# Kernel optimization log

Hardware: AMD Instinct MI355X
Metric: run time of the kernel (lower is better)

The kernel has to match this reference:

```python
import jax, jax.numpy as jnp
import numpy as np

N = 100000      # nodes
E = 1600000     # directed edges (avg degree 16)
F_IN = 256      # dataset.num_node_features
HID = 64        # hidden
C = 40          # dataset.num_classes


def setup_inputs() -> dict:
    key = jax.random.key(0)
    k0, k1, k2, k3 = jax.random.split(key, 4)
    x = jax.random.normal(k0, (N, F_IN), dtype=jnp.float32)
    edge_index = jax.random.randint(k1, (2, E), 0, N, dtype=jnp.int32)
    # Glorot-style init like GCNConv.reset_parameters
    W1 = jax.random.normal(k2, (F_IN, HID), dtype=jnp.float32) * (1.0 / np.sqrt(F_IN))
    b1 = jnp.zeros((HID,), dtype=jnp.float32)
    W2 = jax.random.normal(k3, (HID, C), dtype=jnp.float32) * (1.0 / np.sqrt(HID))
    b2 = jnp.zeros((C,), dtype=jnp.float32)
    return {"x": x, "edge_index": edge_index, "W1": W1, "b1": b1, "W2": W2, "b2": b2}


def gcn_conv(x, row, col, norm, W, b):
    # PyG GCNConv: out[col] += norm * (x @ W)[row]; then + bias
    n = x.shape[0]
    h = x @ W                                   # [N, out]
    msg = h[row] * norm[:, None]                # [E+N, out] gather + scale
    out = jax.ops.segment_sum(msg, col, num_segments=n)  # scatter-add
    return out + b


def _norm_coeffs(edge_index, n, dtype):
    # add self-loops, then symmetric normalization D^{-1/2} A D^{-1/2}
    loop = jnp.arange(n, dtype=edge_index.dtype)
    row = jnp.concatenate([edge_index[0], loop])
    col = jnp.concatenate([edge_index[1], loop])
    deg = jax.ops.segment_sum(jnp.ones_like(col, dtype=dtype), col, num_segments=n)
    dis = jnp.where(deg > 0, jax.lax.rsqrt(jnp.maximum(deg, 1.0)), 0.0)
    return row, col, dis[row] * dis[col]


def reference(x, edge_index, W1, b1, W2, b2):
    n = x.shape[0]
    row, col, norm = _norm_coeffs(edge_index, n, x.dtype)
    h = jax.nn.relu(gcn_conv(x, row, col, norm, W1, b1))
    # F.dropout(p=0.5, training=False) is identity in eval mode
    out = gcn_conv(h, row, col, norm, W2, b2)
    return jax.nn.log_softmax(out, axis=1)
```

## Files before the change

### kernel.cpp

```cpp
#include <hip/hip_runtime.h>
#include <math.h>

#define N_NODES 100000
#define N_EDGES 1600000
#define F_INDIM 256
#define HID 64
#define NCLS 40
#define NBKT 196
#define BKT_CAP 10240
#define EPB 8192

typedef __attribute__((ext_vector_type(8))) short short8;
typedef __attribute__((ext_vector_type(4))) float floatx4;

__device__ __forceinline__ unsigned short f2bf(float f) {
  unsigned u = __float_as_uint(f);
  unsigned r = (u + 0x7FFFu + ((u >> 16) & 1u)) >> 16;
  return (unsigned short)r;
}
__device__ __forceinline__ float bf2f(unsigned short h) {
  return __uint_as_float(((unsigned)h) << 16);
}
__device__ __forceinline__ void add8(float* a, uint4 u) {
  a[0] += __uint_as_float(u.x << 16);
  a[1] += __uint_as_float(u.x & 0xFFFF0000u);
  a[2] += __uint_as_float(u.y << 16);
  a[3] += __uint_as_float(u.y & 0xFFFF0000u);
  a[4] += __uint_as_float(u.z << 16);
  a[5] += __uint_as_float(u.z & 0xFFFF0000u);
  a[6] += __uint_as_float(u.w << 16);
  a[7] += __uint_as_float(u.w & 0xFFFF0000u);
}


__global__ __launch_bounds__(256) void k_zero(int* __restrict__ gcur) {
  int t = threadIdx.x;
  if (t < NBKT) gcur[t] = 0;
}


__global__ __launch_bounds__(256) void k_binA(const int* __restrict__ row,
                                              const int* __restrict__ col,
                                              int* __restrict__ gcur,
                                              unsigned int* __restrict__ bktdata) {
  __shared__ int hist[NBKT];
  __shared__ int cur[NBKT];
  __shared__ int gbase[NBKT];
  const int t = threadIdx.x;
  const int e0 = blockIdx.x * EPB;
  const int n = min(EPB, N_EDGES - e0);
  if (t < NBKT) hist[t] = 0;
  __syncthreads();
  for (int i = t; i < n; i += 256) atomicAdd(&hist[col[e0 + i] >> 9], 1);
  __syncthreads();
  if (t < NBKT) {
    cur[t] = 0;
    int h = hist[t];
    gbase[t] = (h > 0) ? atomicAdd(&gcur[t], h) : 0;
  }
  __syncthreads();
  for (int i = t; i < n; i += 256) {
    int c = col[e0 + i];
    int r = row[e0 + i];
    int b = c >> 9;
    int p = atomicAdd(&cur[b], 1);
    bktdata[(size_t)b * BKT_CAP + gbase[b] + p] =
        ((unsigned)(c & 511) << 17) | (unsigned)r;
  }
}


__global__ __launch_bounds__(256) void k_build2(const int* __restrict__ gcur,
                                                const unsigned int* __restrict__ bktdata,
                                                float* __restrict__ dis,
                                                int* __restrict__ start,
                                                int* __restrict__ esrc) {
  __shared__ int h[512];
  __shared__ int cur[512];
  __shared__ int sbase[512];
  __shared__ int wsum[4];
  const int b = blockIdx.x, t = threadIdx.x;
  h[t] = 0; h[t + 256] = 0; cur[t] = 0; cur[t + 256] = 0;
  int pv = (t < b) ? gcur[t] : 0;
#pragma unroll
  for (int off = 1; off < 64; off <<= 1) pv += __shfl_xor(pv, off);
  if ((t & 63) == 0) wsum[t >> 6] = pv;
  if (b == 0 && t == 0) start[N_NODES] = N_EDGES;
  __syncthreads();
  const int base = wsum[0] + wsum[1] + wsum[2] + wsum[3];

  const int cnt = gcur[b];
  const unsigned int* p = bktdata + (size_t)b * BKT_CAP;
  for (int i = t; i < cnt; i += 256) atomicAdd(&h[p[i] >> 17], 1);
  __syncthreads();

  const int n0 = b * 512 + t, n1 = n0 + 256;
  const int c0 = h[t], c1 = h[t + 256];
  if (n0 < N_NODES) dis[n0] = rsqrtf((float)(c0 + 1));
  if (n1 < N_NODES) dis[n1] = rsqrtf((float)(c1 + 1));
#pragma unroll
  for (int off = 1; off < 512; off <<= 1) {
    int u0 = (t >= off) ? h[t - off] : 0;
    int u1 = ((t + 256) >= off) ? h[t + 256 - off] : 0;
    __syncthreads();
    h[t] += u0; h[t + 256] += u1;
    __syncthreads();
  }
  const int sb0 = base + h[t] - c0;
  const int sb1 = base + h[t + 256] - c1;
  sbase[t] = sb0; sbase[t + 256] = sb1;
  if (n0 < N_NODES) start[n0] = sb0;
  if (n1 < N_NODES) start[n1] = sb1;
  __syncthreads();

  for (int i = t; i < cnt; i += 256) {
    unsigned u = p[i];
    int ld = u >> 17;
    int src = u & 0x1FFFF;
    int pos = sbase[ld] + atomicAdd(&cur[ld], 1);
    esrc[pos] = src;
  }
}


#define KP 264

__global__ __launch_bounds__(256) void k_gemm1(const float* __restrict__ x,
                                               const float* __restrict__ W1,
                                               const float* __restrict__ dis,
                                               unsigned short* __restrict__ h1b) {
  __shared__ unsigned short wt[HID * KP];
  const int tid = threadIdx.x;
  const int lane = tid & 63;
  const int w = tid >> 6;
  const int quad = lane >> 4;
  const int l15 = lane & 15;
  const int rowBase = blockIdx.x * 64;

#pragma unroll
  for (int i = 0; i < 16; ++i) {
    int f = tid + 256 * i;
    int k = f >> 4;
    int n0 = (f & 15) * 4;
    float4 v = *(const float4*)&W1[(size_t)k * HID + n0];
    wt[(n0 + 0) * KP + k] = f2bf(v.x);
    wt[(n0 + 1) * KP + k] = f2bf(v.y);
    wt[(n0 + 2) * KP + k] = f2bf(v.z);
    wt[(n0 + 3) * KP + k] = f2bf(v.w);
  }
  __syncthreads();

  const int ar = rowBase + w * 16 + l15;
  const float* xrow = x + (size_t)((ar < N_NODES) ? ar : N_NODES - 1) * F_INDIM + quad * 8;

  floatx4 acc[4];
#pragma unroll
  for (int c = 0; c < 4; ++c) acc[c] = (floatx4){0.f, 0.f, 0.f, 0.f};

#pragma unroll
  for (int kc = 0; kc < F_INDIM; kc += 32) {
    const float4 va = *(const float4*)(xrow + kc);
    const float4 vb = *(const float4*)(xrow + kc + 4);
    short8 a;
    a[0] = (short)f2bf(va.x); a[1] = (short)f2bf(va.y);
    a[2] = (short)f2bf(va.z); a[3] = (short)f2bf(va.w);
    a[4] = (short)f2bf(vb.x); a[5] = (short)f2bf(vb.y);
    a[6] = (short)f2bf(vb.z); a[7] = (short)f2bf(vb.w);
#pragma unroll
    for (int c = 0; c < 4; ++c) {
      const short8 b = *(const short8*)&wt[(c * 16 + l15) * KP + kc + quad * 8];
      acc[c] = __builtin_amdgcn_mfma_f32_16x16x32_bf16(a, b, acc[c], 0, 0, 0);
    }
  }

#pragma unroll
  for (int reg = 0; reg < 4; ++reg) {
    int gr = rowBase + w * 16 + quad * 4 + reg;
    if (gr < N_NODES) {
      float d = dis[gr];
#pragma unroll
      for (int c = 0; c < 4; ++c)
        h1b[(size_t)gr * HID + c * 16 + l15] = f2bf(d * acc[c][reg]);
    }
  }
}


__global__ __launch_bounds__(256) void k_agg1(const int* __restrict__ esrc,
                                              const int* __restrict__ start,
                                              const float* __restrict__ dis,
                                              const unsigned short* __restrict__ h1b,
                                              const float* __restrict__ b1,
                                              unsigned short* __restrict__ ab) {
  int gid = blockIdx.x * 256 + threadIdx.x;
  int node = gid >> 3;
  int q = gid & 7;
  if (node >= N_NODES) return;
  const uint4* hp4 = (const uint4*)h1b;
  int i = start[node];
  const int e1 = start[node + 1];
  float acc[8];
#pragma unroll
  for (int j = 0; j < 8; ++j) acc[j] = 0.f;
  for (; i + 4 <= e1; i += 4) {
    int s0 = esrc[i];
    int s1 = esrc[i + 1];
    int s2 = esrc[i + 2];
    int s3 = esrc[i + 3];
    uint4 u0 = hp4[(size_t)s0 * 8 + q];
    uint4 u1 = hp4[(size_t)s1 * 8 + q];
    uint4 u2 = hp4[(size_t)s2 * 8 + q];
    uint4 u3 = hp4[(size_t)s3 * 8 + q];
    add8(acc, u0);
    add8(acc, u1);
    add8(acc, u2);
    add8(acc, u3);
  }
  for (; i < e1; ++i) {
    uint4 u = hp4[(size_t)esrc[i] * 8 + q];
    add8(acc, u);
  }
  uint4 us = hp4[(size_t)node * 8 + q];
  add8(acc, us);
  float d = dis[node];
  float4 ba = *(const float4*)&b1[q * 8];
  float4 bb = *(const float4*)&b1[q * 8 + 4];
  float v0 = fmaxf(d * acc[0] + ba.x, 0.f);
  float v1 = fmaxf(d * acc[1] + ba.y, 0.f);
  float v2 = fmaxf(d * acc[2] + ba.z, 0.f);
  float v3 = fmaxf(d * acc[3] + ba.w, 0.f);
  float v4 = fmaxf(d * acc[4] + bb.x, 0.f);
  float v5 = fmaxf(d * acc[5] + bb.y, 0.f);
  float v6 = fmaxf(d * acc[6] + bb.z, 0.f);
  float v7 = fmaxf(d * acc[7] + bb.w, 0.f);
  uint4 o;
  o.x = (unsigned)f2bf(v0) | ((unsigned)f2bf(v1) << 16);
  o.y = (unsigned)f2bf(v2) | ((unsigned)f2bf(v3) << 16);
  o.z = (unsigned)f2bf(v4) | ((unsigned)f2bf(v5) << 16);
  o.w = (unsigned)f2bf(v6) | ((unsigned)f2bf(v7) << 16);
  ((uint4*)ab)[(size_t)node * 8 + q] = o;
}


#define AP 72

__global__ __launch_bounds__(256) void k_gemm2(const unsigned short* __restrict__ ab,
                                               const float* __restrict__ W2,
                                               const float* __restrict__ dis,
                                               unsigned short* __restrict__ gb) {
  __shared__ unsigned short as[64 * AP];
  __shared__ unsigned short w2t[48 * AP];
  const int tid = threadIdx.x;
  const int lane = tid & 63;
  const int w = tid >> 6;
  const int quad = lane >> 4;
  const int l15 = lane & 15;
  const int rowBase = blockIdx.x * 64;

  for (int i = tid; i < 48 * 64; i += 256) {
    int n = i >> 6;
    int k = i & 63;
    w2t[n * AP + k] = (n < NCLS) ? f2bf(W2[(size_t)k * NCLS + n]) : (unsigned short)0;
  }
#pragma unroll
  for (int i = 0; i < 2; ++i) {
    int f = tid + 256 * i;
    int r = f >> 3;
    int q = f & 7;
    int gr = rowBase + r;
    short8 v = (short8){0, 0, 0, 0, 0, 0, 0, 0};
    if (gr < N_NODES) v = *(const short8*)&ab[(size_t)gr * HID + q * 8];
    *(short8*)&as[r * AP + q * 8] = v;
  }
  __syncthreads();

  floatx4 acc[3];
#pragma unroll
  for (int c = 0; c < 3; ++c) acc[c] = (floatx4){0.f, 0.f, 0.f, 0.f};

#pragma unroll
  for (int kh = 0; kh < 2; ++kh) {
    const short8 a = *(const short8*)&as[(w * 16 + l15) * AP + kh * 32 + quad * 8];
#pragma unroll
    for (int c = 0; c < 3; ++c) {
      const short8 b = *(const short8*)&w2t[(c * 16 + l15) * AP + kh * 32 + quad * 8];
      acc[c] = __builtin_amdgcn_mfma_f32_16x16x32_bf16(a, b, acc[c], 0, 0, 0);
    }
  }

#pragma unroll
  for (int reg = 0; reg < 4; ++reg) {
    int gr = rowBase + w * 16 + quad * 4 + reg;
    if (gr < N_NODES) {
      float d = dis[gr];
#pragma unroll
      for (int c = 0; c < 3; ++c) {
        int cc = c * 16 + l15;
        gb[(size_t)gr * 64 + cc] = f2bf(d * acc[c][reg]);
      }
      gb[(size_t)gr * 64 + 48 + l15] = 0;
    }
  }
}


__global__ __launch_bounds__(256) void k_agg2ls(const int* __restrict__ esrc,
                                                const int* __restrict__ start,
                                                const float* __restrict__ dis,
                                                const unsigned short* __restrict__ gb,
                                                const float* __restrict__ b2,
                                                float* __restrict__ out) {
  int gid = blockIdx.x * 256 + threadIdx.x;
  int node = gid >> 3;
  int q = gid & 7;
  if (node >= N_NODES) return;
  const uint4* gp4 = (const uint4*)gb;
  int i = start[node];
  const int e1 = start[node + 1];
  float acc[8];
#pragma unroll
  for (int j = 0; j < 8; ++j) acc[j] = 0.f;
  for (; i + 4 <= e1; i += 4) {
    int s0 = esrc[i];
    int s1 = esrc[i + 1];
    int s2 = esrc[i + 2];
    int s3 = esrc[i + 3];
    uint4 u0 = gp4[(size_t)s0 * 8 + q];
    uint4 u1 = gp4[(size_t)s1 * 8 + q];
    uint4 u2 = gp4[(size_t)s2 * 8 + q];
    uint4 u3 = gp4[(size_t)s3 * 8 + q];
    add8(acc, u0);
    add8(acc, u1);
    add8(acc, u2);
    add8(acc, u3);
  }
  for (; i < e1; ++i) {
    uint4 u = gp4[(size_t)esrc[i] * 8 + q];
    add8(acc, u);
  }
  uint4 us = gp4[(size_t)node * 8 + q];
  add8(acc, us);
  const bool wr = q < 5;
  float v0 = 0.f, v1 = 0.f, v2 = 0.f, v3 = 0.f, v4 = 0.f, v5 = 0.f, v6 = 0.f, v7 = 0.f;
  float m = -INFINITY;
  if (wr) {
    float d = dis[node];
    float4 ba = *(const float4*)&b2[q * 8];
    float4 bb = *(const float4*)&b2[q * 8 + 4];
    v0 = d * acc[0] + ba.x;
    v1 = d * acc[1] + ba.y;
    v2 = d * acc[2] + ba.z;
    v3 = d * acc[3] + ba.w;
    v4 = d * acc[4] + bb.x;
    v5 = d * acc[5] + bb.y;
    v6 = d * acc[6] + bb.z;
    v7 = d * acc[7] + bb.w;
    m = fmaxf(fmaxf(fmaxf(v0, v1), fmaxf(v2, v3)),
              fmaxf(fmaxf(v4, v5), fmaxf(v6, v7)));
  }
#pragma unroll
  for (int off = 1; off < 8; off <<= 1) m = fmaxf(m, __shfl_xor(m, off));
  float el = 0.f;
  if (wr) {
    el = __expf(v0 - m) + __expf(v1 - m) + __expf(v2 - m) + __expf(v3 - m) +
         __expf(v4 - m) + __expf(v5 - m) + __expf(v6 - m) + __expf(v7 - m);
  }
#pragma unroll
  for (int off = 1; off < 8; off <<= 1) el += __shfl_xor(el, off);
  float ls = logf(el);
  if (wr) {
    float4 o1 = make_float4(v0 - m - ls, v1 - m - ls, v2 - m - ls, v3 - m - ls);
    float4 o2 = make_float4(v4 - m - ls, v5 - m - ls, v6 - m - ls, v7 - m - ls);
    *(float4*)&out[(size_t)node * NCLS + q * 8] = o1;
    *(float4*)&out[(size_t)node * NCLS + q * 8 + 4] = o2;
  }
}


extern "C" void kernel_launch(void* const* d_in, const int* in_sizes, int n_in,
                              void* d_out, int out_size, void* d_ws, size_t ws_size,
                              hipStream_t stream) {
  const float* x  = (const float*)d_in[0];
  const int*   ei = (const int*)d_in[1];
  const float* W1 = (const float*)d_in[2];
  const float* b1 = (const float*)d_in[3];
  const float* W2 = (const float*)d_in[4];
  const float* b2 = (const float*)d_in[5];
  float* out = (float*)d_out;

  const int* row = ei;
  const int* col = ei + N_EDGES;

  int*            esrc    = (int*)d_ws;
  unsigned int*   bktdata = (unsigned int*)(esrc + N_EDGES);
  unsigned short* h1b     = (unsigned short*)(bktdata + (size_t)NBKT * BKT_CAP);
  unsigned short* ab      = h1b + (size_t)N_NODES * HID;
  float*          dis     = (float*)(ab + (size_t)N_NODES * HID);
  int*            start   = (int*)(dis + N_NODES);
  int*            gcur    = start + N_NODES + 1;
  unsigned short* gb      = h1b;

  k_zero<<<1, 256, 0, stream>>>(gcur);
  k_binA<<<(N_EDGES + EPB - 1) / EPB, 256, 0, stream>>>(row, col, gcur, bktdata);
  k_build2<<<NBKT, 256, 0, stream>>>(gcur, bktdata, dis, start, esrc);

  k_gemm1<<<(N_NODES + 63) / 64, 256, 0, stream>>>(x, W1, dis, h1b);
  k_agg1<<<(N_NODES * 8 + 255) / 256, 256, 0, stream>>>(esrc, start, dis, h1b, b1, ab);

  k_gemm2<<<(N_NODES + 63) / 64, 256, 0, stream>>>(ab, W2, dis, gb);
  k_agg2ls<<<(N_NODES * 8 + 255) / 256, 256, 0, stream>>>(esrc, start, dis, gb, b2, out);
}
```

Before: 316.3 us.

## Pad CSR neighbor lists to multiples of four with a zero dummy node

Each node's edge list in esrc is padded to a multiple of four, and the pad entries point to an extra zero row appended to the feature buffer. This lets the aggregation kernels read indices as int4 with no scalar tail loop. The edge binning kernel also reads col and row as int4 vectors. The cost is a larger esrc buffer, a separate end-index array, extra gathers of the zero row, and per-bucket padding slack in the offset computation.

```diff
diff --git a/kernel.cpp b/kernel.cpp
--- a/kernel.cpp
+++ b/kernel.cpp
@@ -9,6 +9,7 @@
 #define NBKT 196
 #define BKT_CAP 10240
 #define EPB 8192
+#define ESRC_CAP 1904640
 
 typedef __attribute__((ext_vector_type(8))) short short8;
 typedef __attribute__((ext_vector_type(4))) float floatx4;
@@ -17,9 +18,6 @@
   unsigned u = __float_as_uint(f);
   unsigned r = (u + 0x7FFFu + ((u >> 16) & 1u)) >> 16;
   return (unsigned short)r;
-}
-__device__ __forceinline__ float bf2f(unsigned short h) {
-  return __uint_as_float(((unsigned)h) << 16);
 }
 __device__ __forceinline__ void add8(float* a, uint4 u) {
   a[0] += __uint_as_float(u.x << 16);
@@ -33,9 +31,11 @@
 }
 
 
-__global__ __launch_bounds__(256) void k_zero(int* __restrict__ gcur) {
+__global__ __launch_bounds__(256) void k_zero(int* __restrict__ gcur,
+                                              unsigned int* __restrict__ h1bw) {
   int t = threadIdx.x;
   if (t < NBKT) gcur[t] = 0;
+  if (t < 32) h1bw[(size_t)N_NODES * 32 + t] = 0;
 }
 
 
@@ -51,7 +51,13 @@
   const int n = min(EPB, N_EDGES - e0);
   if (t < NBKT) hist[t] = 0;
   __syncthreads();
-  for (int i = t; i < n; i += 256) atomicAdd(&hist[col[e0 + i] >> 9], 1);
+  for (int i = t * 4; i < n; i += 1024) {
+    int4 c4 = *(const int4*)&col[e0 + i];
+    atomicAdd(&hist[c4.x >> 9], 1);
+    atomicAdd(&hist[c4.y >> 9], 1);
+    atomicAdd(&hist[c4.z >> 9], 1);
+    atomicAdd(&hist[c4.w >> 9], 1);
+  }
   __syncthreads();
   if (t < NBKT) {
     cur[t] = 0;
@@ -59,13 +65,18 @@
     gbase[t] = (h > 0) ? atomicAdd(&gcur[t], h) : 0;
   }
   __syncthreads();
-  for (int i = t; i < n; i += 256) {
-    int c = col[e0 + i];
-    int r = row[e0 + i];
-    int b = c >> 9;
-    int p = atomicAdd(&cur[b], 1);
-    bktdata[(size_t)b * BKT_CAP + gbase[b] + p] =
-        ((unsigned)(c & 511) << 17) | (unsigned)r;
+  for (int i = t * 4; i < n; i += 1024) {
+    int4 c4 = *(const int4*)&col[e0 + i];
+    int4 r4 = *(const int4*)&row[e0 + i];
+#pragma unroll
+    for (int k = 0; k < 4; ++k) {
+      int c = (k == 0) ? c4.x : (k == 1) ? c4.y : (k == 2) ? c4.z : c4.w;
+      int r = (k == 0) ? r4.x : (k == 1) ? r4.y : (k == 2) ? r4.z : r4.w;
+      int b = c >> 9;
+      int p = atomicAdd(&cur[b], 1);
+      bktdata[(size_t)b * BKT_CAP + gbase[b] + p] =
+          ((unsigned)(c & 511) << 17) | (unsigned)r;
+    }
   }
 }
 
@@ -74,6 +85,7 @@
                                                 const unsigned int* __restrict__ bktdata,
                                                 float* __restrict__ dis,
                                                 int* __restrict__ start,
+                                                int* __restrict__ endi,
                                                 int* __restrict__ esrc) {
   __shared__ int h[512];
   __shared__ int cur[512];
@@ -81,11 +93,10 @@
   __shared__ int wsum[4];
   const int b = blockIdx.x, t = threadIdx.x;
   h[t] = 0; h[t + 256] = 0; cur[t] = 0; cur[t + 256] = 0;
-  int pv = (t < b) ? gcur[t] : 0;
+  int pv = (t < b) ? (((gcur[t] + 3) & ~3) + 1536) : 0;
 #pragma unroll
   for (int off = 1; off < 64; off <<= 1) pv += __shfl_xor(pv, off);
   if ((t & 63) == 0) wsum[t >> 6] = pv;
-  if (b == 0 && t == 0) start[N_NODES] = N_EDGES;
   __syncthreads();
   const int base = wsum[0] + wsum[1] + wsum[2] + wsum[3];
 
@@ -96,8 +107,11 @@
 
   const int n0 = b * 512 + t, n1 = n0 + 256;
   const int c0 = h[t], c1 = h[t + 256];
+  const int p0 = (c0 + 3) & ~3, p1 = (c1 + 3) & ~3;
   if (n0 < N_NODES) dis[n0] = rsqrtf((float)(c0 + 1));
   if (n1 < N_NODES) dis[n1] = rsqrtf((float)(c1 + 1));
+  h[t] = p0; h[t + 256] = p1;
+  __syncthreads();
 #pragma unroll
   for (int off = 1; off < 512; off <<= 1) {
     int u0 = (t >= off) ? h[t - off] : 0;
@@ -106,11 +120,13 @@
     h[t] += u0; h[t + 256] += u1;
     __syncthreads();
   }
-  const int sb0 = base + h[t] - c0;
-  const int sb1 = base + h[t + 256] - c1;
+  const int sb0 = base + h[t] - p0;
+  const int sb1 = base + h[t + 256] - p1;
   sbase[t] = sb0; sbase[t + 256] = sb1;
-  if (n0 < N_NODES) start[n0] = sb0;
-  if (n1 < N_NODES) start[n1] = sb1;
+  if (n0 < N_NODES) { start[n0] = sb0; endi[n0] = sb0 + c0; }
+  if (n1 < N_NODES) { start[n1] = sb1; endi[n1] = sb1 + c1; }
+  for (int k = c0; k < p0; ++k) esrc[sb0 + k] = N_NODES;
+  for (int k = c1; k < p1; ++k) esrc[sb1 + k] = N_NODES;
   __syncthreads();
 
   for (int i = t; i < cnt; i += 256) {
@@ -188,6 +204,7 @@
 
 __global__ __launch_bounds__(256) void k_agg1(const int* __restrict__ esrc,
                                               const int* __restrict__ start,
+                                              const int* __restrict__ endi,
                                               const float* __restrict__ dis,
                                               const unsigned short* __restrict__ h1b,
                                               const float* __restrict__ b1,
@@ -197,28 +214,21 @@
   int q = gid & 7;
   if (node >= N_NODES) return;
   const uint4* hp4 = (const uint4*)h1b;
-  int i = start[node];
-  const int e1 = start[node + 1];
+  const int s = start[node];
+  const int epad = (endi[node] + 3) & ~3;
   float acc[8];
 #pragma unroll
   for (int j = 0; j < 8; ++j) acc[j] = 0.f;
-  for (; i + 4 <= e1; i += 4) {
-    int s0 = esrc[i];
-    int s1 = esrc[i + 1];
-    int s2 = esrc[i + 2];
-    int s3 = esrc[i + 3];
-    uint4 u0 = hp4[(size_t)s0 * 8 + q];
-    uint4 u1 = hp4[(size_t)s1 * 8 + q];
-    uint4 u2 = hp4[(size_t)s2 * 8 + q];
-    uint4 u3 = hp4[(size_t)s3 * 8 + q];
+  for (int i = s; i < epad; i += 4) {
+    int4 sv = *(const int4*)&esrc[i];
+    uint4 u0 = hp4[(size_t)sv.x * 8 + q];
+    uint4 u1 = hp4[(size_t)sv.y * 8 + q];
+    uint4 u2 = hp4[(size_t)sv.z * 8 + q];
+    uint4 u3 = hp4[(size_t)sv.w * 8 + q];
     add8(acc, u0);
     add8(acc, u1);
     add8(acc, u2);
     add8(acc, u3);
-  }
-  for (; i < e1; ++i) {
-    uint4 u = hp4[(size_t)esrc[i] * 8 + q];
-    add8(acc, u);
   }
   uint4 us = hp4[(size_t)node * 8 + q];
   add8(acc, us);
@@ -306,6 +316,7 @@
 
 __global__ __launch_bounds__(256) void k_agg2ls(const int* __restrict__ esrc,
                                                 const int* __restrict__ start,
+                                                const int* __restrict__ endi,
                                                 const float* __restrict__ dis,
                                                 const unsigned short* __restrict__ gb,
                                                 const float* __restrict__ b2,
@@ -315,28 +326,21 @@
   int q = gid & 7;
   if (node >= N_NODES) return;
   const uint4* gp4 = (const uint4*)gb;
-  int i = start[node];
-  const int e1 = start[node + 1];
+  const int s = start[node];
+  const int epad = (endi[node] + 3) & ~3;
   float acc[8];
 #pragma unroll
   for (int j = 0; j < 8; ++j) acc[j] = 0.f;
-  for (; i + 4 <= e1; i += 4) {
-    int s0 = esrc[i];
-    int s1 = esrc[i + 1];
-    int s2 = esrc[i + 2];
-    int s3 = esrc[i + 3];
-    uint4 u0 = gp4[(size_t)s0 * 8 + q];
-    uint4 u1 = gp4[(size_t)s1 * 8 + q];
-    uint4 u2 = gp4[(size_t)s2 * 8 + q];
-    uint4 u3 = gp4[(size_t)s3 * 8 + q];
+  for (int i = s; i < epad; i += 4) {
+    int4 sv = *(const int4*)&esrc[i];
+    uint4 u0 = gp4[(size_t)sv.x * 8 + q];
+    uint4 u1 = gp4[(size_t)sv.y * 8 + q];
+    uint4 u2 = gp4[(size_t)sv.z * 8 + q];
+    uint4 u3 = gp4[(size_t)sv.w * 8 + q];
     add8(acc, u0);
     add8(acc, u1);
     add8(acc, u2);
     add8(acc, u3);
-  }
-  for (; i < e1; ++i) {
-    uint4 u = gp4[(size_t)esrc[i] * 8 + q];
-    add8(acc, u);
   }
   uint4 us = gp4[(size_t)node * 8 + q];
   add8(acc, us);
@@ -392,21 +396,22 @@
   const int* col = ei + N_EDGES;
 
   int*            esrc    = (int*)d_ws;
-  unsigned int*   bktdata = (unsigned int*)(esrc + N_EDGES);
+  unsigned int*   bktdata = (unsigned int*)(esrc + ESRC_CAP);
   unsigned short* h1b     = (unsigned short*)(bktdata + (size_t)NBKT * BKT_CAP);
-  unsigned short* ab      = h1b + (size_t)N_NODES * HID;
+  unsigned short* ab      = h1b + (size_t)(N_NODES + 1) * HID;
   float*          dis     = (float*)(ab + (size_t)N_NODES * HID);
   int*            start   = (int*)(dis + N_NODES);
-  int*            gcur    = start + N_NODES + 1;
+  int*            endi    = start + N_NODES + 1;
+  int*            gcur    = endi + N_NODES;
   unsigned short* gb      = h1b;
 
-  k_zero<<<1, 256, 0, stream>>>(gcur);
+  k_zero<<<1, 256, 0, stream>>>(gcur, (unsigned int*)h1b);
   k_binA<<<(N_EDGES + EPB - 1) / EPB, 256, 0, stream>>>(row, col, gcur, bktdata);
-  k_build2<<<NBKT, 256, 0, stream>>>(gcur, bktdata, dis, start, esrc);
+  k_build2<<<NBKT, 256, 0, stream>>>(gcur, bktdata, dis, start, endi, esrc);
 
   k_gemm1<<<(N_NODES + 63) / 64, 256, 0, stream>>>(x, W1, dis, h1b);
-  k_agg1<<<(N_NODES * 8 + 255) / 256, 256, 0, stream>>>(esrc, start, dis, h1b, b1, ab);
+  k_agg1<<<(N_NODES * 8 + 255) / 256, 256, 0, stream>>>(esrc, start, endi, dis, h1b, b1, ab);
 
   k_gemm2<<<(N_NODES + 63) / 64, 256, 0, stream>>>(ab, W2, dis, gb);
-  k_agg2ls<<<(N_NODES * 8 + 255) / 256, 256, 0, stream>>>(esrc, start, dis, gb, b2, out);
-}
+  k_agg2ls<<<(N_NODES * 8 + 255) / 256, 256, 0, stream>>>(esrc, start, endi, dis, gb, b2, out);
+}
```

Measured after the change: 304.3 us. 3.8% less time.
